# Optimization experiments

Measured on AMD Instinct MI355X. Metric: run time of the kernel, lower is better.

## Reference

```python
import jax, jax.numpy as jnp
import numpy as np

B, T, D, H = 2, 1024, 1024, 16
WINDOW = 32
KSZ = 2 * WINDOW + 1
MAXG = 32


def setup_inputs() -> dict:
    key = jax.random.key(0)
    ks = jax.random.split(key, 5)
    s = 0.02
    x = jax.random.normal(ks[0], (B, T, D), jnp.float32)
    Wq = jax.random.normal(ks[1], (D, D), jnp.float32) * s
    Wk = jax.random.normal(ks[2], (D, D), jnp.float32) * s
    Wv = jax.random.normal(ks[3], (D, D), jnp.float32) * s
    Wo = jax.random.normal(ks[4], (D, D), jnp.float32) * s
    # global tokens: one every T//MAXG positions (same for every batch row)
    global_mask = jnp.tile((jnp.arange(T) % (T // MAXG) == 0)[None, :], (B, 1))
    return {"x": x, "global_mask": global_mask, "Wq": Wq, "Wk": Wk,
            "Wv": Wv, "Wo": Wo, "maxG": MAXG}


def reference(x, global_mask, Wq, Wk, Wv, Wo, maxG):
    Bb, Tt, Dm = x.shape
    dh = Dm // H
    scale = dh ** -0.5

    def proj(W):
        return (x @ W.T).reshape(Bb, Tt, H, dh).transpose(0, 2, 1, 3)  # (B,H,T,dh)

    q, k, v = proj(Wq), proj(Wk), proj(Wv)

    # sliding windows via zero-padded gather (== F.unfold with padding=WINDOW)
    widx = jnp.arange(Tt)[:, None] + jnp.arange(KSZ)[None, :]  # index into padded axis

    def windows(t):
        tp = jnp.pad(t, ((0, 0), (0, 0), (WINDOW, WINDOW), (0, 0)))
        return tp[:, :, widx, :]  # (B,H,T,KSZ,dh)

    Kw, Vw = windows(k), windows(v)
    scores_local = jnp.einsum('bhtd,bhtwd->bhtw', q, Kw) * scale

    # pack global-token indices (stable argsort puts True positions first, in order)
    order = jnp.argsort(jnp.logical_not(global_mask), axis=1, stable=True)
    gidx = order[:, :maxG]                                   # (B,maxG)
    gvalid = jnp.take_along_axis(global_mask, gidx, axis=1)  # (B,maxG) bool
    gather_b = jax.vmap(lambda arr, i: arr[:, i, :])         # (H,T,dh),(maxG,)->(H,maxG,dh)
    Kg = gather_b(k, gidx) * gvalid[:, None, :, None]
    Vg = gather_b(v, gidx) * gvalid[:, None, :, None]

    scores_global = jnp.einsum('bhtd,bhgd->bhtg', q, Kg) * scale
    scores_global = jnp.where(gvalid[:, None, None, :], scores_global, -1e9)

    attn = jax.nn.softmax(jnp.concatenate([scores_local, scores_global], axis=-1), axis=-1)
    wl, wg = attn[..., :KSZ], attn[..., KSZ:]
    ctx = (jnp.einsum('bhtw,bhtwd->bhtd', wl, Vw)
           + jnp.einsum('bhtg,bhgd->bhtd', wg, Vg))
    out = ctx.transpose(0, 2, 1, 3).reshape(Bb, Tt, Dm) @ Wo.T

    # ---- debug full attention map (vectorized replica of the per-token loop) ----
    t = jnp.arange(Tt)
    left = jnp.maximum(0, t - WINDOW)
    win_len = jnp.minimum(Tt, t + WINDOW + 1) - left           # (T,)
    valid_w = jnp.arange(KSZ)[None, :] < win_len[:, None]      # (T,KSZ)
    s_loc = jnp.where(valid_w[None, None], scores_local, -jnp.inf)
    attn_d = jax.nn.softmax(jnp.concatenate([s_loc, scores_global], axis=-1), axis=-1)
    wl_d = attn_d[..., :KSZ] * valid_w[None, None]             # (B,H,T,KSZ)
    wg_d = attn_d[..., KSZ:] * gvalid[:, None, None, :]        # (B,H,T,maxG)
    cols = jnp.minimum(left[:, None] + jnp.arange(KSZ)[None, :], Tt - 1)  # (T,KSZ)
    rows = jnp.broadcast_to(t[:, None], (Tt, KSZ))
    full_attn = jnp.zeros((Bb, H, Tt, Tt), x.dtype)
    full_attn = full_attn.at[:, :, rows, cols].add(wl_d)
    full_attn = jax.vmap(lambda fa, w, gi: fa.at[:, :, gi].add(w))(full_attn, wg_d, gidx)
    return out, full_attn
```

## Files before the change

kernel.cpp:

```cpp
#include <hip/hip_runtime.h>

#define T_   1024
#define B_   2
#define H_   16
#define DH   64
#define D_   1024
#define WND  32
#define KSZ  65
#define NG   32

typedef float f32x4 __attribute__((ext_vector_type(4)));
typedef __bf16 bf16x8 __attribute__((ext_vector_type(8)));
typedef __bf16 bf16x4 __attribute__((ext_vector_type(4)));
typedef unsigned short u16x4 __attribute__((ext_vector_type(4)));

__device__ __forceinline__ unsigned short f2bf(float f) {
  unsigned u = __float_as_uint(f);
  return (unsigned short)((u + 0x7fffu + ((u >> 16) & 1u)) >> 16);
}

__device__ __forceinline__ void gload16(const unsigned short* g, unsigned short* l) {
  __builtin_amdgcn_global_load_lds(
      (const __attribute__((address_space(1))) unsigned int*)g,
      (__attribute__((address_space(3))) unsigned int*)l, 16, 0, 0);
}

__global__ __launch_bounds__(256) void cvt_kernel(const float* __restrict__ x,
    const float* __restrict__ wq, const float* __restrict__ wk,
    const float* __restrict__ wv, const float* __restrict__ wo,
    unsigned short* __restrict__ dst,
    const int* __restrict__ mask, int* __restrict__ gidxo, float* __restrict__ gvalo) {
  if (blockIdx.x == 6144) {
    if (threadIdx.x < 128) {
      int b = threadIdx.x >> 6, lane = threadIdx.x & 63;
      const int* mb = mask + b * T_;
      unsigned long long lanemask = (1ull << lane) - 1ull;
      int base = 0;
      for (int c = 0; c < 16 && base < NG; ++c) {
        int t = c * 64 + lane;
        bool m = mb[t] != 0;
        unsigned long long bal = __ballot(m);
        int rank = __popcll(bal & lanemask);
        if (m && base + rank < NG) { gidxo[b*NG+base+rank] = t; gvalo[b*NG+base+rank] = 1.f; }
        base += __popcll(bal);
      }
      if (base < NG) {
        for (int c = 0; c < 16 && base < NG; ++c) {
          int t = c * 64 + lane;
          bool m = mb[t] == 0;
          unsigned long long bal = __ballot(m);
          int rank = __popcll(bal & lanemask);
          if (m && base + rank < NG) { gidxo[b*NG+base+rank] = t; gvalo[b*NG+base+rank] = 0.f; }
          base += __popcll(bal);
        }
      }
    }
    return;
  }
  int idx = (blockIdx.x * 256 + threadIdx.x) * 4;
  int r = idx >> 20;
  const float* src; int off;
  if (r < 2)       { src = x;  off = idx; }
  else if (r == 2) { src = wq; off = idx - 2 * 1048576; }
  else if (r == 3) { src = wk; off = idx - 3 * 1048576; }
  else if (r == 4) { src = wv; off = idx - 4 * 1048576; }
  else             { src = wo; off = idx - 5 * 1048576; }
  f32x4 v = *(const f32x4*)(src + off);
  u16x4 o;
  o.x = f2bf(v[0]); o.y = f2bf(v[1]); o.z = f2bf(v[2]); o.w = f2bf(v[3]);
  *(u16x4*)(dst + idx) = o;
}

template<int MODE, int BM, int BK, bool GLDS>
__global__ __launch_bounds__(256) void gemm128(const unsigned short* __restrict__ A,
    const unsigned short* __restrict__ B0, const unsigned short* __restrict__ B1,
    const unsigned short* __restrict__ B2,
    void* __restrict__ C0v, void* __restrict__ C1v, void* __restrict__ C2v) {
  constexpr int K = 1024;
  constexpr int FM = BM / 32;
  constexpr int WM = BM / 2;
  constexpr int CPR = BK / 8;
  constexpr int AIT = BM * CPR / 256;
  constexpr int BIT = 128 * CPR / 256;
  __shared__ __attribute__((aligned(16))) unsigned short SMEM[BM * BK + 128 * BK];
  unsigned short* As = SMEM;
  unsigned short* Bs = SMEM + BM * BK;

  int m0 = blockIdx.x * BM, n0 = blockIdx.y * 128;
  int zz = (MODE == 0) ? blockIdx.z : 0;
  const unsigned short* Bb = (MODE == 0) ? (zz == 0 ? B0 : (zz == 1 ? B1 : B2)) : B0;

  int tid = threadIdx.x;
  int w = tid >> 6, l = tid & 63;
  int wr = w >> 1, wc = w & 1;
  int lr = l & 15, kg = l >> 4;

  f32x4 acc[FM][4] = {};

  for (int kt = 0; kt < K; kt += BK) {
    __syncthreads();
    if constexpr (GLDS) {
#pragma unroll
      for (int i = 0; i < AIT; ++i) {
        int ci = tid + 256 * i;
        int row = ci / CPR, c8 = (ci % CPR) ^ (row & 7);
        gload16(A + (size_t)(m0 + row) * K + kt + c8 * 8, As + ci * 8);
      }
#pragma unroll
      for (int i = 0; i < BIT; ++i) {
        int ci = tid + 256 * i;
        int row = ci / CPR, c8 = (ci % CPR) ^ (row & 7);
        gload16(Bb + (size_t)(n0 + row) * K + kt + c8 * 8, Bs + ci * 8);
      }
    } else {
#pragma unroll
      for (int i = 0; i < AIT; ++i) {
        int ci = tid + 256 * i;
        int row = ci / CPR, c8 = ci % CPR;
        *(bf16x8*)&As[row * BK + ((c8 ^ (row & 7)) * 8)] =
            *(const bf16x8*)&A[(size_t)(m0 + row) * K + kt + c8 * 8];
      }
#pragma unroll
      for (int i = 0; i < BIT; ++i) {
        int ci = tid + 256 * i;
        int row = ci / CPR, c8 = ci % CPR;
        *(bf16x8*)&Bs[row * BK + ((c8 ^ (row & 7)) * 8)] =
            *(const bf16x8*)&Bb[(size_t)(n0 + row) * K + kt + c8 * 8];
      }
    }
    __syncthreads();
#pragma unroll
    for (int kk = 0; kk < BK / 32; ++kk) {
      int c8 = kk * 4 + kg;
      bf16x8 af[FM], bfr[4];
#pragma unroll
      for (int mi = 0; mi < FM; ++mi) {
        int row = wr * WM + mi * 16 + lr;
        af[mi] = *(bf16x8*)&As[row * BK + (((c8 ^ (row & 7))) * 8)];
      }
#pragma unroll
      for (int ni = 0; ni < 4; ++ni) {
        int row = wc * 64 + ni * 16 + lr;
        bfr[ni] = *(bf16x8*)&Bs[row * BK + (((c8 ^ (row & 7))) * 8)];
      }
#pragma unroll
      for (int mi = 0; mi < FM; ++mi)
#pragma unroll
        for (int ni = 0; ni < 4; ++ni)
          acc[mi][ni] = __builtin_amdgcn_mfma_f32_16x16x32_bf16(af[mi], bfr[ni], acc[mi][ni], 0, 0, 0);
    }
  }

  if (MODE == 1) {
    float* C = (float*)C0v;
#pragma unroll
    for (int mi = 0; mi < FM; ++mi)
#pragma unroll
      for (int ni = 0; ni < 4; ++ni) {
        int mbase = m0 + wr * WM + mi * 16 + (l >> 4) * 4;
        int n = n0 + wc * 64 + ni * 16 + lr;
#pragma unroll
        for (int r = 0; r < 4; ++r)
          C[(size_t)(mbase + r) * 1024 + n] = acc[mi][ni][r];
      }
  } else if (zz < 2) {
    unsigned short* C = (unsigned short*)(zz == 0 ? C0v : C1v);
#pragma unroll
    for (int mi = 0; mi < FM; ++mi)
#pragma unroll
      for (int ni = 0; ni < 4; ++ni) {
        int mbase = m0 + wr * WM + mi * 16 + (l >> 4) * 4;
        int n = n0 + wc * 64 + ni * 16 + lr;
#pragma unroll
        for (int r = 0; r < 4; ++r) {
          __bf16 v = (__bf16)acc[mi][ni][r];
          C[(size_t)(mbase + r) * 1024 + n] = *(unsigned short*)&v;
        }
      }
  } else {
    constexpr int RS = BM * 2;
    constexpr int TCH = BM / 8;
    constexpr int NIT = 128 * TCH / 256;
    __syncthreads();
    char* Tb = (char*)SMEM;
#pragma unroll
    for (int mi = 0; mi < FM; ++mi)
#pragma unroll
      for (int ni = 0; ni < 4; ++ni) {
        int mb2 = wr * WM + mi * 16 + (l >> 4) * 4;
        int nl = wc * 64 + ni * 16 + lr;
        bf16x4 pk;
        pk[0] = (__bf16)acc[mi][ni][0]; pk[1] = (__bf16)acc[mi][ni][1];
        pk[2] = (__bf16)acc[mi][ni][2]; pk[3] = (__bf16)acc[mi][ni][3];
        *(bf16x4*)(Tb + ((nl * RS + mb2 * 2) ^ ((nl & 7) << 4))) = pk;
      }
    __syncthreads();
    unsigned short* C = (unsigned short*)C2v;
    int bb = m0 >> 10, tbase = m0 & 1023;
#pragma unroll
    for (int it = 0; it < NIT; ++it) {
      int ci = tid + 256 * it;
      int dl = ci / TCH, tc = ci % TCH;
      bf16x8 v = *(bf16x8*)(Tb + ((dl * RS + tc * 16) ^ ((dl & 7) << 4)));
      int n = n0 + dl, hh = n >> 6, dd = n & 63;
      *(bf16x8*)&C[((size_t)(bb * H_ + hh) * DH + dd) * T_ + tbase + tc * 8] = v;
    }
  }
}

__global__ __launch_bounds__(512, 4) void attn_kernel(
    const unsigned short* __restrict__ qg, const unsigned short* __restrict__ kg_,
    const unsigned short* __restrict__ vg,
    const int* __restrict__ gidx_g, const float* __restrict__ gval_g,
    unsigned short* __restrict__ ctxb, float* __restrict__ fa) {
  int tid = threadIdx.x;
  int lid = blockIdx.x + 32 * blockIdx.y + 512 * blockIdx.z;
  int swz = (lid & 7) * 128 + (lid >> 3);
  int b = swz >> 9, h = (swz >> 5) & 15;
  int t0 = (swz & 31) * 32;
  int lane = tid & 63, wv = tid >> 6;

  __shared__ __attribute__((aligned(16))) unsigned short QbL[32 * 64];
  __shared__ __attribute__((aligned(16))) unsigned short KbL[128 * 64];
  __shared__ __attribute__((aligned(16))) unsigned short VtL[64 * 128];
  __shared__ __attribute__((aligned(16))) unsigned short WbL[32 * 128];
  __shared__ __attribute__((aligned(16))) float Sf[32][132];
  __shared__ float m_out_s[32], invdo_s[32], rowfac_s[32];
  __shared__ int   gidx_s[32];
  __shared__ float gval_s[32];

  if (tid < 32) { gidx_s[tid] = gidx_g[b * NG + tid]; gval_s[tid] = gval_g[b * NG + tid]; }
  ((unsigned long long*)WbL)[tid] = 0ull;
  ((unsigned long long*)WbL)[tid + 512] = 0ull;
  __syncthreads();

  const unsigned short* qbh = qg + (size_t)(b * T_ + t0) * D_ + h * DH;
  const unsigned short* kbh = kg_ + (size_t)(b * T_) * D_ + h * DH;
  const unsigned short* vbh = vg + (size_t)(b * H_ + h) * DH * T_;

  if (tid < 256) {
    int r = tid >> 3, c8 = tid & 7;
    bf16x8 v = *(const bf16x8*)(qbh + (size_t)r * D_ + c8 * 8);
    *(bf16x8*)((char*)QbL + ((r * 128 + c8 * 16) ^ ((r & 7) << 4))) = v;
  }
#pragma unroll
  for (int it = 0; it < 2; ++it) {
    int fi = tid + it * 512;
    int r = fi >> 3, c8 = fi & 7;
    int col; bool valid;
    if (r < 96) { col = t0 - 32 + r; valid = (col >= 0 && col < T_); }
    else { int g = r - 96; valid = gval_s[g] > 0.f; col = valid ? gidx_s[g] : 0; }
    bf16x8 v = {};
    if (valid) v = *(const bf16x8*)(kbh + (size_t)col * D_ + c8 * 8);
    *(bf16x8*)((char*)KbL + ((r * 128 + c8 * 16) ^ ((r & 7) << 4))) = v;
  }
#pragma unroll
  for (int it = 0; it < 2; ++it) {
    int fi = tid + it * 512;
    if (fi < 768) {
      int d = fi / 12, rc = fi % 12;
      int cb = t0 - 32 + rc * 8;
      bf16x8 v = {};
      if (cb >= 0 && cb < T_) v = *(const bf16x8*)(vbh + d * T_ + cb);
      *(bf16x8*)((char*)VtL + ((d * 256 + rc * 16) ^ ((d & 7) << 4))) = v;
    }
  }
#pragma unroll
  for (int it = 0; it < 4; ++it) {
    int fi = tid + it * 512;
    int d = fi >> 5, g = fi & 31;
    unsigned short v = 0;
    if (gval_s[g] > 0.f) v = vbh[d * T_ + gidx_s[g]];
    *(unsigned short*)((char*)VtL + ((d * 256 + (96 + g) * 2) ^ ((d & 7) << 4))) = v;
  }
  __syncthreads();

  {
    int mt = wv & 1, nq = wv >> 1;
    int lrr = lane & 15, kgl = lane >> 4;
    int arow = mt * 16 + lrr;
    f32x4 acc0 = {}, acc1 = {};
#pragma unroll
    for (int s = 0; s < 2; ++s) {
      int c = s * 4 + kgl;
      bf16x8 a = *(bf16x8*)((char*)QbL + ((arow * 128 + c * 16) ^ ((arow & 7) << 4)));
      int br0 = nq * 32 + lrr, br1 = nq * 32 + 16 + lrr;
      bf16x8 b0 = *(bf16x8*)((char*)KbL + ((br0 * 128 + c * 16) ^ ((br0 & 7) << 4)));
      bf16x8 b1 = *(bf16x8*)((char*)KbL + ((br1 * 128 + c * 16) ^ ((br1 & 7) << 4)));
      acc0 = __builtin_amdgcn_mfma_f32_16x16x32_bf16(a, b0, acc0, 0, 0, 0);
      acc1 = __builtin_amdgcn_mfma_f32_16x16x32_bf16(a, b1, acc1, 0, 0, 0);
    }
    int orow = mt * 16 + (lane >> 4) * 4;
#pragma unroll
    for (int i = 0; i < 4; ++i) {
      Sf[orow + i][nq * 32 + lrr] = acc0[i] * 0.125f;
      Sf[orow + i][nq * 32 + 16 + lrr] = acc1[i] * 0.125f;
    }
  }
  __syncthreads();

  {
    int r = tid >> 4, lg = tid & 15;
    int t_abs = t0 + r;
    int left = (t_abs - WND > 0) ? (t_abs - WND) : 0;
    int tmp = t_abs + WND + 1; if (tmp > T_) tmp = T_;
    int wl = tmp - left;
    float sv[8]; bool vld[8], vdd[8];
#pragma unroll
    for (int ii = 0; ii < 8; ++ii) {
      int c = lg + ii * 16;
      bool loc = (c >= r && c <= r + 64);
      bool glob = (c >= 96);
      float s = Sf[r][c];
      if (glob && !(gval_s[c - 96] > 0.f)) s = -1e9f;
      vld[ii] = loc || glob;
      vdd[ii] = loc ? ((c - r) < wl) : glob;
      sv[ii] = s;
    }
    float mo = -1e30f, md = -1e30f;
#pragma unroll
    for (int ii = 0; ii < 8; ++ii) {
      if (vld[ii]) mo = fmaxf(mo, sv[ii]);
      if (vdd[ii]) md = fmaxf(md, sv[ii]);
    }
#pragma unroll
    for (int o = 1; o < 16; o <<= 1) {
      mo = fmaxf(mo, __shfl_xor(mo, o, 16));
      md = fmaxf(md, __shfl_xor(md, o, 16));
    }
    float eo = 0.f, ed = 0.f;
#pragma unroll
    for (int ii = 0; ii < 8; ++ii) {
      if (vld[ii]) eo += __expf(sv[ii] - mo);
      if (vdd[ii]) ed += __expf(sv[ii] - md);
    }
#pragma unroll
    for (int o = 1; o < 16; o <<= 1) {
      eo += __shfl_xor(eo, o, 16);
      ed += __shfl_xor(ed, o, 16);
    }
    if (lg == 0) {
      m_out_s[r] = mo;
      invdo_s[r] = 1.f / eo;
      rowfac_s[r] = (eo / ed) * __expf(mo - md);
    }
  }
  __syncthreads();

  for (int idx = tid; idx < 32 * 97; idx += 512) {
    int t = idx / 97;
    int j = idx - t * 97;
    int cc = (j < KSZ) ? (t + j) : (j + 31);
    float s = Sf[t][cc];
    float wgt = __expf(s - m_out_s[t]) * invdo_s[t];
    Sf[t][cc] = wgt;
    *(unsigned short*)((char*)WbL + ((t * 256 + cc * 2) ^ ((t & 7) << 4))) = f2bf(wgt);
  }
  __syncthreads();

  {
    int mt = wv >> 1, nt = wv & 1;
    int lrr = lane & 15, kgl = lane >> 4;
    int arow = mt * 16 + lrr;
    int brow = nt * 16 + lrr;
    f32x4 acc = {};
#pragma unroll
    for (int s = 0; s < 4; ++s) {
      int c = s * 4 + kgl;
      bf16x8 a = *(bf16x8*)((char*)VtL + ((arow * 256 + c * 16) ^ ((arow & 7) << 4)));
      bf16x8 bb = *(bf16x8*)((char*)WbL + ((brow * 256 + c * 16) ^ ((brow & 7) << 4)));
      acc = __builtin_amdgcn_mfma_f32_16x16x32_bf16(a, bb, acc, 0, 0, 0);
    }
    int t = nt * 16 + lrr;
    int dbase = mt * 16 + (lane >> 4) * 4;
    u16x4 st;
    st.x = f2bf(acc[0]); st.y = f2bf(acc[1]); st.z = f2bf(acc[2]); st.w = f2bf(acc[3]);
    *(u16x4*)(ctxb + ((size_t)(b * T_ + t0 + t)) * D_ + h * DH + dbase) = st;
  }

  {
    int rp = tid >> 8;
    int c0 = (tid & 255) * 4;
    unsigned gm = 0;
#pragma unroll
    for (int g = 0; g < NG; ++g) {
      int gc = gidx_s[g];
      if (gval_s[g] > 0.f && gc >= c0 && gc < c0 + 4) gm |= (1u << g);
    }
#pragma unroll 2
    for (int rr = 0; rr < 16; ++rr) {
      int r = rr * 2 + rp;
      int t_abs = t0 + r;
      int left = (t_abs - WND > 0) ? (t_abs - WND) : 0;
      int tmp = t_abs + WND + 1; if (tmp > T_) tmp = T_;
      int wl = tmp - left;
      float rf = rowfac_s[r];
      f32x4 o = {0.f, 0.f, 0.f, 0.f};
      int jj0 = c0 - left;
      if (jj0 > -4 && jj0 < wl) {
#pragma unroll
        for (int e = 0; e < 4; ++e) {
          int jj = jj0 + e;
          if (jj >= 0 && jj < wl) o[e] = Sf[r][r + jj] * rf;
        }
      }
      if (gm) {
        unsigned mm = gm;
        while (mm) {
          int g = __ffs(mm) - 1; mm &= mm - 1;
          o[gidx_s[g] - c0] += Sf[r][96 + g] * rf;
        }
      }
      float* dst = fa + (((size_t)(b * H_ + h) * T_) + t_abs) * T_ + c0;
      *(f32x4*)dst = o;
    }
  }
}

extern "C" void kernel_launch(void* const* d_in, const int* in_sizes, int n_in,
                              void* d_out, int out_size, void* d_ws, size_t ws_size,
                              hipStream_t stream) {
  const float* x   = (const float*)d_in[0];
  const int* gmask = (const int*)d_in[1];
  const float* wq  = (const float*)d_in[2];
  const float* wk  = (const float*)d_in[3];
  const float* wv  = (const float*)d_in[4];
  const float* wo  = (const float*)d_in[5];

  unsigned short* arena = (unsigned short*)d_ws;
  unsigned short* xb  = arena;
  unsigned short* wqb = arena + 2 * 1048576;
  unsigned short* wkb = arena + 3 * 1048576;
  unsigned short* wvb = arena + 4 * 1048576;
  unsigned short* wob = arena + 5 * 1048576;
  unsigned short* qb   = arena + 6 * 1048576;
  unsigned short* kb   = arena + 8 * 1048576;
  unsigned short* vtb  = arena + 10 * 1048576;
  unsigned short* ctxb = arena + 12 * 1048576;
  int*   gidx = (int*)(arena + 14 * 1048576);
  float* gval = (float*)(gidx + 64);

  float* outp = (float*)d_out;
  float* fa   = outp + 2097152;

  cvt_kernel<<<dim3(6145), dim3(256), 0, stream>>>(x, wq, wk, wv, wo, xb, gmask, gidx, gval);
  gemm128<0, 64, 128, true><<<dim3(32, 8, 3), dim3(256), 0, stream>>>(xb, wqb, wkb, wvb, qb, kb, vtb);
  attn_kernel<<<dim3(32, 16, 2), dim3(512), 0, stream>>>(qb, kb, vtb, gidx, gval, ctxb, fa);
  gemm128<1, 64, 64, false><<<dim3(32, 8, 1), dim3(256), 0, stream>>>(ctxb, wob, wob, wob, outp, outp, outp);
}
```

Baseline: 87.41 us.

## Alias score buffer onto K tile LDS and add dedicated 64x64 output GEMM

The attention kernel's separate 32x132 float score buffer is removed. Scores are now stored in the K-tile LDS region, which is dead after QK^T, using an XOR-swizzled index, and an extra barrier protects the reuse. The smaller LDS footprint lets launch bounds ask for 6 blocks per CU instead of 4. The output projection moves to a new 64x64-tile GEMM that uses direct global-to-LDS loads and launches twice as many blocks, trading per-block reuse for more parallelism.

```diff
diff --git a/kernel.cpp b/kernel.cpp
--- a/kernel.cpp
+++ b/kernel.cpp
@@ -24,6 +24,8 @@
       (const __attribute__((address_space(1))) unsigned int*)g,
       (__attribute__((address_space(3))) unsigned int*)l, 16, 0, 0);
 }
+
+#define SFIDX(r, c) ((r) * 128 + ((c) ^ (((r) & 7) << 3)))
 
 __global__ __launch_bounds__(256) void cvt_kernel(const float* __restrict__ x,
     const float* __restrict__ wq, const float* __restrict__ wk,
@@ -71,7 +73,7 @@
   *(u16x4*)(dst + idx) = o;
 }
 
-template<int MODE, int BM, int BK, bool GLDS>
+template<int BM, int BK>
 __global__ __launch_bounds__(256) void gemm128(const unsigned short* __restrict__ A,
     const unsigned short* __restrict__ B0, const unsigned short* __restrict__ B1,
     const unsigned short* __restrict__ B2,
@@ -87,8 +89,8 @@
   unsigned short* Bs = SMEM + BM * BK;
 
   int m0 = blockIdx.x * BM, n0 = blockIdx.y * 128;
-  int zz = (MODE == 0) ? blockIdx.z : 0;
-  const unsigned short* Bb = (MODE == 0) ? (zz == 0 ? B0 : (zz == 1 ? B1 : B2)) : B0;
+  int zz = blockIdx.z;
+  const unsigned short* Bb = (zz == 0 ? B0 : (zz == 1 ? B1 : B2));
 
   int tid = threadIdx.x;
   int w = tid >> 6, l = tid & 63;
@@ -99,34 +101,17 @@
 
   for (int kt = 0; kt < K; kt += BK) {
     __syncthreads();
-    if constexpr (GLDS) {
-#pragma unroll
-      for (int i = 0; i < AIT; ++i) {
-        int ci = tid + 256 * i;
-        int row = ci / CPR, c8 = (ci % CPR) ^ (row & 7);
-        gload16(A + (size_t)(m0 + row) * K + kt + c8 * 8, As + ci * 8);
-      }
-#pragma unroll
-      for (int i = 0; i < BIT; ++i) {
-        int ci = tid + 256 * i;
-        int row = ci / CPR, c8 = (ci % CPR) ^ (row & 7);
-        gload16(Bb + (size_t)(n0 + row) * K + kt + c8 * 8, Bs + ci * 8);
-      }
-    } else {
-#pragma unroll
-      for (int i = 0; i < AIT; ++i) {
-        int ci = tid + 256 * i;
-        int row = ci / CPR, c8 = ci % CPR;
-        *(bf16x8*)&As[row * BK + ((c8 ^ (row & 7)) * 8)] =
-            *(const bf16x8*)&A[(size_t)(m0 + row) * K + kt + c8 * 8];
-      }
-#pragma unroll
-      for (int i = 0; i < BIT; ++i) {
-        int ci = tid + 256 * i;
-        int row = ci / CPR, c8 = ci % CPR;
-        *(bf16x8*)&Bs[row * BK + ((c8 ^ (row & 7)) * 8)] =
-            *(const bf16x8*)&Bb[(size_t)(n0 + row) * K + kt + c8 * 8];
-      }
+#pragma unroll
+    for (int i = 0; i < AIT; ++i) {
+      int ci = tid + 256 * i;
+      int row = ci / CPR, c8 = (ci % CPR) ^ (row & 7);
+      gload16(A + (size_t)(m0 + row) * K + kt + c8 * 8, As + ci * 8);
+    }
+#pragma unroll
+    for (int i = 0; i < BIT; ++i) {
+      int ci = tid + 256 * i;
+      int row = ci / CPR, c8 = (ci % CPR) ^ (row & 7);
+      gload16(Bb + (size_t)(n0 + row) * K + kt + c8 * 8, Bs + ci * 8);
     }
     __syncthreads();
 #pragma unroll
@@ -151,19 +136,7 @@
     }
   }
 
-  if (MODE == 1) {
-    float* C = (float*)C0v;
-#pragma unroll
-    for (int mi = 0; mi < FM; ++mi)
-#pragma unroll
-      for (int ni = 0; ni < 4; ++ni) {
-        int mbase = m0 + wr * WM + mi * 16 + (l >> 4) * 4;
-        int n = n0 + wc * 64 + ni * 16 + lr;
-#pragma unroll
-        for (int r = 0; r < 4; ++r)
-          C[(size_t)(mbase + r) * 1024 + n] = acc[mi][ni][r];
-      }
-  } else if (zz < 2) {
+  if (zz < 2) {
     unsigned short* C = (unsigned short*)(zz == 0 ? C0v : C1v);
 #pragma unroll
     for (int mi = 0; mi < FM; ++mi)
@@ -208,7 +181,71 @@
   }
 }
 
-__global__ __launch_bounds__(512, 4) void attn_kernel(
+__global__ __launch_bounds__(256) void out_gemm(const unsigned short* __restrict__ A,
+    const unsigned short* __restrict__ Bw, float* __restrict__ C) {
+  constexpr int K = 1024;
+  __shared__ __attribute__((aligned(16))) unsigned short SMEM[64 * 64 * 2];
+  unsigned short* As = SMEM;
+  unsigned short* Bs = SMEM + 64 * 64;
+
+  int m0 = blockIdx.x * 64, n0 = blockIdx.y * 64;
+  int tid = threadIdx.x;
+  int w = tid >> 6, l = tid & 63;
+  int wr = w >> 1, wc = w & 1;
+  int lr = l & 15, kg = l >> 4;
+
+  f32x4 acc[2][2] = {};
+
+  for (int kt = 0; kt < K; kt += 64) {
+    __syncthreads();
+#pragma unroll
+    for (int i = 0; i < 2; ++i) {
+      int ci = tid + 256 * i;
+      int row = ci >> 3, c8 = (ci & 7) ^ (row & 7);
+      gload16(A + (size_t)(m0 + row) * K + kt + c8 * 8, As + ci * 8);
+    }
+#pragma unroll
+    for (int i = 0; i < 2; ++i) {
+      int ci = tid + 256 * i;
+      int row = ci >> 3, c8 = (ci & 7) ^ (row & 7);
+      gload16(Bw + (size_t)(n0 + row) * K + kt + c8 * 8, Bs + ci * 8);
+    }
+    __syncthreads();
+#pragma unroll
+    for (int kk = 0; kk < 2; ++kk) {
+      int c8 = kk * 4 + kg;
+      bf16x8 af[2], bfr[2];
+#pragma unroll
+      for (int mi = 0; mi < 2; ++mi) {
+        int row = wr * 32 + mi * 16 + lr;
+        af[mi] = *(bf16x8*)&As[row * 64 + ((c8 ^ (row & 7)) * 8)];
+      }
+#pragma unroll
+      for (int ni = 0; ni < 2; ++ni) {
+        int row = wc * 32 + ni * 16 + lr;
+        bfr[ni] = *(bf16x8*)&Bs[row * 64 + ((c8 ^ (row & 7)) * 8)];
+      }
+#pragma unroll
+      for (int mi = 0; mi < 2; ++mi)
+#pragma unroll
+        for (int ni = 0; ni < 2; ++ni)
+          acc[mi][ni] = __builtin_amdgcn_mfma_f32_16x16x32_bf16(af[mi], bfr[ni], acc[mi][ni], 0, 0, 0);
+    }
+  }
+
+#pragma unroll
+  for (int mi = 0; mi < 2; ++mi)
+#pragma unroll
+    for (int ni = 0; ni < 2; ++ni) {
+      int mbase = m0 + wr * 32 + mi * 16 + (l >> 4) * 4;
+      int n = n0 + wc * 32 + ni * 16 + lr;
+#pragma unroll
+      for (int r = 0; r < 4; ++r)
+        C[(size_t)(mbase + r) * 1024 + n] = acc[mi][ni][r];
+    }
+}
+
+__global__ __launch_bounds__(512, 6) void attn_kernel(
     const unsigned short* __restrict__ qg, const unsigned short* __restrict__ kg_,
     const unsigned short* __restrict__ vg,
     const int* __restrict__ gidx_g, const float* __restrict__ gval_g,
@@ -224,10 +261,10 @@
   __shared__ __attribute__((aligned(16))) unsigned short KbL[128 * 64];
   __shared__ __attribute__((aligned(16))) unsigned short VtL[64 * 128];
   __shared__ __attribute__((aligned(16))) unsigned short WbL[32 * 128];
-  __shared__ __attribute__((aligned(16))) float Sf[32][132];
   __shared__ float m_out_s[32], invdo_s[32], rowfac_s[32];
   __shared__ int   gidx_s[32];
   __shared__ float gval_s[32];
+  float* Sfp = (float*)KbL;
 
   if (tid < 32) { gidx_s[tid] = gidx_g[b * NG + tid]; gval_s[tid] = gval_g[b * NG + tid]; }
   ((unsigned long long*)WbL)[tid] = 0ull;
@@ -290,11 +327,12 @@
       acc0 = __builtin_amdgcn_mfma_f32_16x16x32_bf16(a, b0, acc0, 0, 0, 0);
       acc1 = __builtin_amdgcn_mfma_f32_16x16x32_bf16(a, b1, acc1, 0, 0, 0);
     }
+    __syncthreads();
     int orow = mt * 16 + (lane >> 4) * 4;
 #pragma unroll
     for (int i = 0; i < 4; ++i) {
-      Sf[orow + i][nq * 32 + lrr] = acc0[i] * 0.125f;
-      Sf[orow + i][nq * 32 + 16 + lrr] = acc1[i] * 0.125f;
+      Sfp[SFIDX(orow + i, nq * 32 + lrr)] = acc0[i] * 0.125f;
+      Sfp[SFIDX(orow + i, nq * 32 + 16 + lrr)] = acc1[i] * 0.125f;
     }
   }
   __syncthreads();
@@ -311,7 +349,7 @@
       int c = lg + ii * 16;
       bool loc = (c >= r && c <= r + 64);
       bool glob = (c >= 96);
-      float s = Sf[r][c];
+      float s = Sfp[SFIDX(r, c)];
       if (glob && !(gval_s[c - 96] > 0.f)) s = -1e9f;
       vld[ii] = loc || glob;
       vdd[ii] = loc ? ((c - r) < wl) : glob;
@@ -351,9 +389,9 @@
     int t = idx / 97;
     int j = idx - t * 97;
     int cc = (j < KSZ) ? (t + j) : (j + 31);
-    float s = Sf[t][cc];
+    float s = Sfp[SFIDX(t, cc)];
     float wgt = __expf(s - m_out_s[t]) * invdo_s[t];
-    Sf[t][cc] = wgt;
+    Sfp[SFIDX(t, cc)] = wgt;
     *(unsigned short*)((char*)WbL + ((t * 256 + cc * 2) ^ ((t & 7) << 4))) = f2bf(wgt);
   }
   __syncthreads();
@@ -401,14 +439,14 @@
 #pragma unroll
         for (int e = 0; e < 4; ++e) {
           int jj = jj0 + e;
-          if (jj >= 0 && jj < wl) o[e] = Sf[r][r + jj] * rf;
+          if (jj >= 0 && jj < wl) o[e] = Sfp[SFIDX(r, r + jj)] * rf;
         }
       }
       if (gm) {
         unsigned mm = gm;
         while (mm) {
           int g = __ffs(mm) - 1; mm &= mm - 1;
-          o[gidx_s[g] - c0] += Sf[r][96 + g] * rf;
+          o[gidx_s[g] - c0] += Sfp[SFIDX(r, 96 + g)] * rf;
         }
       }
       float* dst = fa + (((size_t)(b * H_ + h) * T_) + t_abs) * T_ + c0;
@@ -444,7 +482,7 @@
   float* fa   = outp + 2097152;
 
   cvt_kernel<<<dim3(6145), dim3(256), 0, stream>>>(x, wq, wk, wv, wo, xb, gmask, gidx, gval);
-  gemm128<0, 64, 128, true><<<dim3(32, 8, 3), dim3(256), 0, stream>>>(xb, wqb, wkb, wvb, qb, kb, vtb);
+  gemm128<64, 128><<<dim3(32, 8, 3), dim3(256), 0, stream>>>(xb, wqb, wkb, wvb, qb, kb, vtb);
   attn_kernel<<<dim3(32, 16, 2), dim3(512), 0, stream>>>(qb, kb, vtb, gidx, gval, ctxb, fa);
-  gemm128<1, 64, 64, false><<<dim3(32, 8, 1), dim3(256), 0, stream>>>(ctxb, wob, wob, wob, outp, outp, outp);
-}
+  out_gemm<<<dim3(32, 16), dim3(256), 0, stream>>>(ctxb, wob, outp);
+}
```

After: 86.70 us. No clear change (-0.8%).
